# Kernel optimization log

Hardware: AMD Instinct MI355X
Metric: run time of the kernel (lower is better)

Reference implementation:

```python
import jax, jax.numpy as jnp
import numpy as np

EPS = 1e-6


def bbox_ciou(box1, box2):
    # box*: [..., 4] in (cx, cy, w, h); broadcasts like the torch version
    b1_x1, b1_y1 = box1[..., 0] - box1[..., 2] / 2, box1[..., 1] - box1[..., 3] / 2
    b1_x2, b1_y2 = box1[..., 0] + box1[..., 2] / 2, box1[..., 1] + box1[..., 3] / 2
    b2_x1, b2_y1 = box2[..., 0] - box2[..., 2] / 2, box2[..., 1] - box2[..., 3] / 2
    b2_x2, b2_y2 = box2[..., 0] + box2[..., 2] / 2, box2[..., 1] + box2[..., 3] / 2
    inter_w = jnp.clip(jnp.minimum(b1_x2, b2_x2) - jnp.maximum(b1_x1, b2_x1), 0)
    inter_h = jnp.clip(jnp.minimum(b1_y2, b2_y2) - jnp.maximum(b1_y1, b2_y1), 0)
    inter_area = inter_w * inter_h
    b1_area = (b1_x2 - b1_x1) * (b1_y2 - b1_y1)
    b2_area = (b2_x2 - b2_x1) * (b2_y2 - b2_y1)
    union = b1_area + b2_area - inter_area
    iou = inter_area / (union + EPS)
    center_dist = (box1[..., 0] - box2[..., 0]) ** 2 + (box1[..., 1] - box2[..., 1]) ** 2
    enc_w = jnp.maximum(b1_x2, b2_x2) - jnp.minimum(b1_x1, b2_x1)
    enc_h = jnp.maximum(b1_y2, b2_y2) - jnp.minimum(b1_y1, b2_y1)
    enc_diag = enc_w ** 2 + enc_h ** 2
    v = (4.0 / np.pi ** 2) * (jnp.arctan(box1[..., 2] / box1[..., 3])
                              - jnp.arctan(box2[..., 2] / box2[..., 3])) ** 2
    alpha = v / (1 - iou + v + EPS)  # no stop-gradient in the original
    return iou - center_dist / (enc_diag + EPS) - alpha * v


def setup_inputs() -> dict:
    key = jax.random.key(0)
    k1, k2, k3 = jax.random.split(key, 3)
    B, N, D, G, C = 64, 25200, 21, 32, 16
    preds = jax.random.uniform(k1, (B, N, D), dtype=jnp.float32)
    # keep w,h strictly positive (atan(w/h) division) as real box preds would be
    gt_boxes = jax.random.uniform(k2, (B, G, 4), minval=0.05, maxval=1.0, dtype=jnp.float32)
    gt_cls = jax.random.randint(k3, (B, G), 0, C, dtype=jnp.int32)
    return {"preds": preds, "gt_boxes": gt_boxes, "gt_cls": gt_cls}


def reference(preds, gt_boxes, gt_cls):
    lambda_cls, lambda_obj, lambda_box = 1.0, 1.0, 5.0
    # match: CIoU of every pred box vs every GT -> [B, G, N]
    pred_boxes = preds[..., :4]
    ious = bbox_ciou(pred_boxes[:, None, :, :], gt_boxes[:, :, None, :])
    best_idx = jnp.argmax(ious, axis=-1)  # [B, G]
    matched = jnp.take_along_axis(preds, best_idx[..., None], axis=1)  # [B, G, 5+C]
    ciou = bbox_ciou(matched[..., :4], gt_boxes)  # [B, G]
    loss_box = jnp.sum(1.0 - ciou)
    # BCEWithLogits with target 1 on a scalar logit == softplus(-logit)
    loss_obj = jnp.sum(jax.nn.softplus(-matched[..., 4]))
    cls_logit = jnp.take_along_axis(matched[..., 5:], gt_cls[..., None].astype(jnp.int32), axis=-1)[..., 0]
    loss_cls = jnp.sum(jax.nn.softplus(-cls_logit))
    return lambda_box * loss_box + lambda_obj * loss_obj + lambda_cls * loss_cls
```

## Files before the change

### kernel.cpp

```cpp
#include <hip/hip_runtime.h>
#include <math.h>

#ifndef INFINITY
#define INFINITY __builtin_inff()
#endif

#define EPS 1e-6f
#define K4PI2 0.405284734569351086f

constexpr int B = 64;
constexpr int N = 25200;
constexpr int D = 21;
constexpr int G = 32;
constexpr int CHUNKS = 16;
constexpr int CHUNK = N / CHUNKS;
constexpr int BLK = 512;
constexpr int TILE = 512;
constexpr int NW = BLK / 64;
constexpr int STREAMS = NW * 2;

typedef float f32x4u __attribute__((ext_vector_type(4), aligned(4)));

__device__ __forceinline__ float fastrcp(float x) {
    return __builtin_amdgcn_rcpf(x);
}

__device__ __forceinline__ float softplusf(float x) {
    return fmaxf(x, 0.0f) + log1pf(expf(-fabsf(x)));
}

__device__ __forceinline__ float ciou_exact(float p_cx, float p_cy, float pw, float ph,
                                            float g_cx, float g_cy, float gw, float gh) {
    float p_x1 = p_cx - pw * 0.5f, p_y1 = p_cy - ph * 0.5f;
    float p_x2 = p_cx + pw * 0.5f, p_y2 = p_cy + ph * 0.5f;
    float g_x1 = g_cx - gw * 0.5f, g_y1 = g_cy - gh * 0.5f;
    float g_x2 = g_cx + gw * 0.5f, g_y2 = g_cy + gh * 0.5f;
    float iw = fmaxf(fminf(p_x2, g_x2) - fmaxf(p_x1, g_x1), 0.0f);
    float ih = fmaxf(fminf(p_y2, g_y2) - fmaxf(p_y1, g_y1), 0.0f);
    float inter = iw * ih;
    float p_area = (p_x2 - p_x1) * (p_y2 - p_y1);
    float g_area = (g_x2 - g_x1) * (g_y2 - g_y1);
    float uni = p_area + g_area - inter;
    float iou = inter / (uni + EPS);
    float dx = p_cx - g_cx, dy = p_cy - g_cy;
    float cd = dx * dx + dy * dy;
    float ew = fmaxf(p_x2, g_x2) - fminf(p_x1, g_x1);
    float eh = fmaxf(p_y2, g_y2) - fminf(p_y1, g_y1);
    float ed = ew * ew + eh * eh;
    float dat = atanf(pw / ph) - atanf(gw / gh);
    float v = K4PI2 * (dat * dat);
    float alpha = v / (1.0f - iou + v + EPS);
    return iou - cd / (ed + EPS) - alpha * v;
}

__global__ __launch_bounds__(BLK, 6) void k_argmax(const float* __restrict__ preds,
                                                   const float* __restrict__ gt_boxes,
                                                   float* __restrict__ pval,
                                                   int* __restrict__ pidx) {
    __shared__ float4 sA[TILE];
    __shared__ float4 sB[TILE];
    __shared__ float2 sC[TILE];
    __shared__ float rv[NW][G];
    __shared__ int ri[NW][G];

    const int b = blockIdx.x / CHUNKS;
    const int chunk = blockIdx.x % CHUNKS;
    const int tid = threadIdx.x;
    const int lane = tid & 63;
    const int wid = tid >> 6;
    const int g = lane & 31;
    const int stream = wid * 2 + (lane >> 5);

    const float4 gt4 = *reinterpret_cast<const float4*>(gt_boxes + ((size_t)b * G + g) * 4);
    const float gcx = gt4.x, gcy = gt4.y;
    const float gx1 = gcx - gt4.z * 0.5f, gy1 = gcy - gt4.w * 0.5f;
    const float gx2 = gcx + gt4.z * 0.5f, gy2 = gcy + gt4.w * 0.5f;
    const float gww = gx2 - gx1, ghh = gy2 - gy1;
    const float garea = gww * ghh;
    const float gat = atanf(gt4.z / gt4.w);

    float bestv = -INFINITY;
    int besti = 0x7fffffff;

    const int n0 = chunk * CHUNK;
    const float qnan = __builtin_nanf("");

    for (int t0 = 0; t0 < CHUNK; t0 += TILE) {
        {
            const int p = t0 + tid;
            if (p < CHUNK) {
                const int n = n0 + p;
                const f32x4u pr =
                    *reinterpret_cast<const f32x4u*>(preds + ((size_t)b * N + n) * D);
                float cx = pr.x, cy = pr.y, w = pr.z, h = pr.w;
                float px1 = cx - w * 0.5f, py1 = cy - h * 0.5f;
                float px2 = cx + w * 0.5f, py2 = cy + h * 0.5f;
                float pw = px2 - px1, ph = py2 - py1;
                sA[tid] = make_float4(px1, py1, px2, py2);
                sB[tid] = make_float4(pw, ph, pw * ph + EPS, atanf(w / h));
                sC[tid] = make_float2(cx, cy);
            } else {
                sA[tid] = make_float4(qnan, qnan, qnan, qnan);
                sB[tid] = make_float4(qnan, qnan, qnan, qnan);
                sC[tid] = make_float2(qnan, qnan);
            }
        }
        __syncthreads();

        const int nbase = n0 + t0;
#pragma unroll 8
        for (int it = 0; it < TILE / STREAMS; ++it) {
            const int pp = it * STREAMS + stream;
            const float4 A = sA[pp];
            const float4 Bv = sB[pp];
            const float2 C2 = sC[pp];
            float iw = fminf(A.z, gx2) - fmaxf(A.x, gx1);
            float ih = fminf(A.w, gy2) - fmaxf(A.y, gy1);
            float inter = fmaxf(iw, 0.0f) * fmaxf(ih, 0.0f);
            float uni = (garea + Bv.z) - inter;
            float iou = inter * fastrcp(uni);
            float dx = C2.x - gcx, dy = C2.y - gcy;
            float cd = dx * dx + dy * dy;
            float ew = (Bv.x + gww) - iw;
            float eh = (Bv.y + ghh) - ih;
            float ed = ew * ew + eh * eh + EPS;
            float dat = Bv.w - gat;
            float v = K4PI2 * (dat * dat);
            float den = (1.0f + EPS) + v - iou;
            float ciou = iou - cd * fastrcp(ed) - (v * v) * fastrcp(den);
            if (ciou > bestv) { bestv = ciou; besti = nbase + pp; }
        }
        __syncthreads();
    }

    {
        float ov = __shfl_down(bestv, 32);
        int oi = __shfl_down(besti, 32);
        if (ov > bestv || (ov == bestv && oi < besti)) { bestv = ov; besti = oi; }
        if (lane < 32) { rv[wid][g] = bestv; ri[wid][g] = besti; }
    }
    __syncthreads();

    if (tid < G) {
        float v = rv[0][tid];
        int i = ri[0][tid];
#pragma unroll
        for (int w = 1; w < NW; ++w) {
            float ov = rv[w][tid];
            int oi = ri[w][tid];
            if (ov > v || (ov == v && oi < i)) { v = ov; i = oi; }
        }
        size_t o = ((size_t)b * G + tid) * CHUNKS + chunk;
        pval[o] = v;
        pidx[o] = i;
    }
}

__global__ __launch_bounds__(64) void k_loss(const float* __restrict__ preds,
                                             const float* __restrict__ gt_boxes,
                                             const int* __restrict__ gt_cls,
                                             const float* __restrict__ pval,
                                             const int* __restrict__ pidx,
                                             float* __restrict__ partial) {
    const int b = blockIdx.x;
    const int tid = threadIdx.x;
    float contrib = 0.0f;
    if (tid < G) {
        const int g = tid;
        size_t base = ((size_t)b * G + g) * CHUNKS;
        float v = pval[base];
        int i = pidx[base];
#pragma unroll
        for (int c = 1; c < CHUNKS; ++c) {
            float ov = pval[base + c];
            int oi = pidx[base + c];
            if (ov > v || (ov == v && oi < i)) { v = ov; i = oi; }
        }
        const float* pr = preds + ((size_t)b * N + i) * D;
        const f32x4u p4 = *reinterpret_cast<const f32x4u*>(pr);
        const float* gb = gt_boxes + ((size_t)b * G + g) * 4;
        float ciou = ciou_exact(p4.x, p4.y, p4.z, p4.w, gb[0], gb[1], gb[2], gb[3]);
        float loss_box = 1.0f - ciou;
        float loss_obj = softplusf(-pr[4]);
        int cls = gt_cls[b * G + g];
        float loss_cls = softplusf(-pr[5 + cls]);
        contrib = 5.0f * loss_box + loss_obj + loss_cls;
    }
#pragma unroll
    for (int off = 32; off > 0; off >>= 1) contrib += __shfl_down(contrib, off);
    if (tid == 0) partial[b] = contrib;
}

__global__ __launch_bounds__(64) void k_final(const float* __restrict__ partial,
                                              float* __restrict__ out) {
    float v = partial[threadIdx.x];
#pragma unroll
    for (int off = 32; off > 0; off >>= 1) v += __shfl_down(v, off);
    if (threadIdx.x == 0) out[0] = v;
}

extern "C" void kernel_launch(void* const* d_in, const int* in_sizes, int n_in,
                              void* d_out, int out_size, void* d_ws, size_t ws_size,
                              hipStream_t stream) {
    const float* preds = (const float*)d_in[0];
    const float* gt_boxes = (const float*)d_in[1];
    const int* gt_cls = (const int*)d_in[2];
    float* out = (float*)d_out;

    float* pval = (float*)d_ws;
    int* pidx = (int*)((char*)d_ws + sizeof(float) * (size_t)B * G * CHUNKS);
    float* partial = (float*)((char*)d_ws + 2 * sizeof(float) * (size_t)B * G * CHUNKS);

    k_argmax<<<B * CHUNKS, BLK, 0, stream>>>(preds, gt_boxes, pval, pidx);
    k_loss<<<B, 64, 0, stream>>>(preds, gt_boxes, gt_cls, pval, pidx, partial);
    k_final<<<1, 64, 0, stream>>>(partial, out);
}
```

Baseline: 239.6 us.

## Double-buffer pred tiles in LDS and prefetch next tile during compute

The argmax kernel now keeps two LDS buffers and issues the global load for the next tile before computing the current one, transforming and storing it afterwards. This removes one of the two barriers per tile and hides global load latency. It also packs the per-pred data into two float4s instead of three arrays, recomputes the enclosing box with min/max instead of stored widths, and trims the inner loop on the partial last tile. LDS use per block grows slightly, which may reduce occupancy.

```diff
diff --git a/kernel.cpp b/kernel.cpp
--- a/kernel.cpp
+++ b/kernel.cpp
@@ -18,6 +18,7 @@
 constexpr int TILE = 512;
 constexpr int NW = BLK / 64;
 constexpr int STREAMS = NW * 2;
+constexpr int NTILES = (CHUNK + TILE - 1) / TILE;
 
 typedef float f32x4u __attribute__((ext_vector_type(4), aligned(4)));
 
@@ -57,9 +58,7 @@
                                                    const float* __restrict__ gt_boxes,
                                                    float* __restrict__ pval,
                                                    int* __restrict__ pidx) {
-    __shared__ float4 sA[TILE];
-    __shared__ float4 sB[TILE];
-    __shared__ float2 sC[TILE];
+    __shared__ float4 sP[2][TILE * 2];
     __shared__ float rv[NW][G];
     __shared__ int ri[NW][G];
 
@@ -70,65 +69,89 @@
     const int wid = tid >> 6;
     const int g = lane & 31;
     const int stream = wid * 2 + (lane >> 5);
+    const int n0 = chunk * CHUNK;
+    const float qnan = __builtin_nanf("");
 
     const float4 gt4 = *reinterpret_cast<const float4*>(gt_boxes + ((size_t)b * G + g) * 4);
     const float gcx = gt4.x, gcy = gt4.y;
     const float gx1 = gcx - gt4.z * 0.5f, gy1 = gcy - gt4.w * 0.5f;
     const float gx2 = gcx + gt4.z * 0.5f, gy2 = gcy + gt4.w * 0.5f;
-    const float gww = gx2 - gx1, ghh = gy2 - gy1;
-    const float garea = gww * ghh;
+    const float garea = (gx2 - gx1) * (gy2 - gy1);
     const float gat = atanf(gt4.z / gt4.w);
 
     float bestv = -INFINITY;
     int besti = 0x7fffffff;
 
-    const int n0 = chunk * CHUNK;
-    const float qnan = __builtin_nanf("");
-
-    for (int t0 = 0; t0 < CHUNK; t0 += TILE) {
-        {
-            const int p = t0 + tid;
+    {
+        const int p = tid;
+        if (p < CHUNK) {
+            const f32x4u pr =
+                *reinterpret_cast<const f32x4u*>(preds + ((size_t)b * N + n0 + p) * D);
+            float cx = pr.x, cy = pr.y, w = pr.z, h = pr.w;
+            float px1 = cx - w * 0.5f, py1 = cy - h * 0.5f;
+            float px2 = cx + w * 0.5f, py2 = cy + h * 0.5f;
+            sP[0][2 * tid] = make_float4(px1, py1, px2, py2);
+            sP[0][2 * tid + 1] =
+                make_float4((px2 - px1) * (py2 - py1) + EPS, atanf(w / h), cx, cy);
+        } else {
+            sP[0][2 * tid] = make_float4(qnan, qnan, qnan, qnan);
+            sP[0][2 * tid + 1] = make_float4(qnan, qnan, qnan, qnan);
+        }
+    }
+    __syncthreads();
+
+    for (int k = 0; k < NTILES; ++k) {
+        const int t0 = k * TILE;
+        const int buf = k & 1;
+
+        f32x4u raw;
+        bool have = false;
+        if (k + 1 < NTILES) {
+            const int p = t0 + TILE + tid;
             if (p < CHUNK) {
-                const int n = n0 + p;
-                const f32x4u pr =
-                    *reinterpret_cast<const f32x4u*>(preds + ((size_t)b * N + n) * D);
-                float cx = pr.x, cy = pr.y, w = pr.z, h = pr.w;
-                float px1 = cx - w * 0.5f, py1 = cy - h * 0.5f;
-                float px2 = cx + w * 0.5f, py2 = cy + h * 0.5f;
-                float pw = px2 - px1, ph = py2 - py1;
-                sA[tid] = make_float4(px1, py1, px2, py2);
-                sB[tid] = make_float4(pw, ph, pw * ph + EPS, atanf(w / h));
-                sC[tid] = make_float2(cx, cy);
-            } else {
-                sA[tid] = make_float4(qnan, qnan, qnan, qnan);
-                sB[tid] = make_float4(qnan, qnan, qnan, qnan);
-                sC[tid] = make_float2(qnan, qnan);
+                raw = *reinterpret_cast<const f32x4u*>(preds + ((size_t)b * N + n0 + p) * D);
+                have = true;
             }
         }
-        __syncthreads();
-
+
+        const int navail = (CHUNK - t0 < TILE) ? (CHUNK - t0) : TILE;
+        const int iters = (navail + STREAMS - 1) / STREAMS;
         const int nbase = n0 + t0;
-#pragma unroll 8
-        for (int it = 0; it < TILE / STREAMS; ++it) {
+#pragma unroll 4
+        for (int it = 0; it < iters; ++it) {
             const int pp = it * STREAMS + stream;
-            const float4 A = sA[pp];
-            const float4 Bv = sB[pp];
-            const float2 C2 = sC[pp];
+            const float4 A = sP[buf][2 * pp];
+            const float4 Q = sP[buf][2 * pp + 1];
             float iw = fminf(A.z, gx2) - fmaxf(A.x, gx1);
             float ih = fminf(A.w, gy2) - fmaxf(A.y, gy1);
             float inter = fmaxf(iw, 0.0f) * fmaxf(ih, 0.0f);
-            float uni = (garea + Bv.z) - inter;
+            float uni = (garea + Q.x) - inter;
             float iou = inter * fastrcp(uni);
-            float dx = C2.x - gcx, dy = C2.y - gcy;
+            float dx = Q.z - gcx, dy = Q.w - gcy;
             float cd = dx * dx + dy * dy;
-            float ew = (Bv.x + gww) - iw;
-            float eh = (Bv.y + ghh) - ih;
+            float ew = fmaxf(A.z, gx2) - fminf(A.x, gx1);
+            float eh = fmaxf(A.w, gy2) - fminf(A.y, gy1);
             float ed = ew * ew + eh * eh + EPS;
-            float dat = Bv.w - gat;
+            float dat = Q.y - gat;
             float v = K4PI2 * (dat * dat);
             float den = (1.0f + EPS) + v - iou;
             float ciou = iou - cd * fastrcp(ed) - (v * v) * fastrcp(den);
             if (ciou > bestv) { bestv = ciou; besti = nbase + pp; }
+        }
+
+        if (k + 1 < NTILES) {
+            const int nb = buf ^ 1;
+            if (have) {
+                float cx = raw.x, cy = raw.y, w = raw.z, h = raw.w;
+                float px1 = cx - w * 0.5f, py1 = cy - h * 0.5f;
+                float px2 = cx + w * 0.5f, py2 = cy + h * 0.5f;
+                sP[nb][2 * tid] = make_float4(px1, py1, px2, py2);
+                sP[nb][2 * tid + 1] =
+                    make_float4((px2 - px1) * (py2 - py1) + EPS, atanf(w / h), cx, cy);
+            } else {
+                sP[nb][2 * tid] = make_float4(qnan, qnan, qnan, qnan);
+                sP[nb][2 * tid + 1] = make_float4(qnan, qnan, qnan, qnan);
+            }
         }
         __syncthreads();
     }
```

Result: faster. 223.6 us (-6.7%).
